# Kernel optimization log

Hardware: AMD Instinct MI355X
Metric: run time of the kernel (lower is better)

## Reference

```python
import jax, jax.numpy as jnp
import numpy as np

B, T, D, H = 8, 4096, 1024, 1024


def log_g(x):
    # log of g(x) = relu(x)+0.5 for x>=0, sigmoid(x) for x<0 (continuous at 0)
    return jnp.where(x >= 0, jnp.log(jax.nn.relu(x) + 0.5), -jax.nn.softplus(-x))


def setup_inputs() -> dict:
    key = jax.random.key(0)
    k0, k1, k2, k3, k4, k5 = jax.random.split(key, 6)
    s = 1.0 / np.sqrt(D)
    return {
        "x": jax.random.normal(k0, (B, T, D), jnp.float32),
        "h_0": jax.random.normal(k1, (B, H), jnp.float32),
        "Wz": jax.random.uniform(k2, (H, D), jnp.float32, -s, s),
        "bz": jax.random.uniform(k3, (H,), jnp.float32, -s, s),
        "Wh": jax.random.uniform(k4, (H, D), jnp.float32, -s, s),
        "bh": jax.random.uniform(k5, (H,), jnp.float32, -s, s),
    }


def reference(x, h_0, Wz, bz, Wh, bh):
    # gate pre-activation k: (B,T,H)
    k = jnp.einsum("btd,hd->bth", x, Wz) + bz
    log_z = -jax.nn.softplus(-k)        # log sigmoid(k)
    log_coeffs = -jax.nn.softplus(k)    # log (1 - sigmoid(k))
    log_h_0 = log_g(h_0)[:, None, :]    # (B,1,H)
    log_tilde_h = log_g(jnp.einsum("btd,hd->bth", x, Wh) + bh)
    log_values = jnp.concatenate([log_h_0, log_z + log_tilde_h], axis=1)  # (B,T+1,H)
    # parallel scan in log space
    a_star = jnp.pad(jnp.cumsum(log_coeffs, axis=1), ((0, 0), (1, 0), (0, 0)))
    log_h = a_star + jax.lax.cumlogsumexp(log_values - a_star, axis=1)
    h = jnp.exp(log_h)                  # (B,T+1,H)
    return h[:, -T:, :]
```

## Files before the change

kernel.cpp:

```cpp
#include <hip/hip_runtime.h>
#include <hip/hip_bf16.h>

#define Bb 8
#define Tt 4096
#define Dd 1024
#define Hh 1024
#define Mm (Bb * Tt)
#define NCHUNK 32
#define CLEN 128

typedef float f32x4 __attribute__((ext_vector_type(4)));
typedef short bf16x8 __attribute__((ext_vector_type(8)));

__device__ __forceinline__ unsigned f2bfu(float x) {
  unsigned u = __float_as_uint(x);
  return (u + 0x7fffu + ((u >> 16) & 1u)) >> 16;
}
__device__ __forceinline__ float bflo(unsigned u) { return __uint_as_float(u << 16); }
__device__ __forceinline__ float bfhi(unsigned u) { return __uint_as_float(u & 0xffff0000u); }

__global__ void cvt_kernel(const float* __restrict__ src, unsigned short* __restrict__ dst,
                           int n4) {
  int i = blockIdx.x * blockDim.x + threadIdx.x;
  int stride = gridDim.x * blockDim.x;
  for (; i < n4; i += stride) {
    float4 v = reinterpret_cast<const float4*>(src)[i];
    ushort4 o;
    o.x = (unsigned short)f2bfu(v.x);
    o.y = (unsigned short)f2bfu(v.y);
    o.z = (unsigned short)f2bfu(v.z);
    o.w = (unsigned short)f2bfu(v.w);
    reinterpret_cast<ushort4*>(dst)[i] = o;
  }
}

__device__ __forceinline__ void async16(const unsigned short* g, unsigned short* l) {
  __builtin_amdgcn_global_load_lds(
      (const __attribute__((address_space(1))) unsigned int*)g,
      (__attribute__((address_space(3))) unsigned int*)l, 16, 0, 0);
}

template <int MF0>
__device__ __forceinline__ void mfma16(const bf16x8 af[4], const bf16x8 bfr[4],
                                       f32x4 (&acc)[8][4]) {
#pragma unroll
  for (int i = 0; i < 4; ++i)
#pragma unroll
    for (int j = 0; j < 4; ++j)
      acc[MF0 + i][j] =
          __builtin_amdgcn_mfma_f32_16x16x32_bf16(af[i], bfr[j], acc[MF0 + i][j], 0, 0, 0);
}

__global__ void __launch_bounds__(512, 1) gemm_kernel(
    const unsigned short* __restrict__ xb,
    const unsigned short* __restrict__ wzb,
    const unsigned short* __restrict__ whb,
    const float* __restrict__ bz,
    const float* __restrict__ bh,
    unsigned int* __restrict__ P) {
  __shared__ unsigned short lds[65536];
  const int tid = threadIdx.x;
  const int wid = tid >> 6;
  const int wm = wid >> 2;
  const int wn = wid & 3;
  const int l = tid & 63, ln = l & 15, l4 = l >> 4;

  const int id = blockIdx.x;
  const int sw = (id & 7) * 128 + (id >> 3);
  const int mb = sw >> 3, nb = sw & 7;
  const int m0 = mb * 256, h0 = nb * 128;

  const int r0 = tid >> 2;
  const int chunk = ((tid & 3) - (tid >> 3)) & 3;
  const unsigned short* agp = xb + (size_t)(m0 + r0) * Dd + chunk * 8;
  const int sub16 = r0 >> 4;
  const int hrow0 = h0 + ((sub16 >> 1) << 4) + (r0 & 15);
  const unsigned short* bgp =
      ((sub16 & 1) ? whb : wzb) + (size_t)hrow0 * Dd + chunk * 8;
  const int dstoff = tid * 8;

  auto stA = [&](int reg) {
    unsigned short* d = &lds[reg * 8192] + dstoff;
    async16(agp, d);
    async16(agp + (size_t)128 * Dd, d + 4096);
    agp += 32;
  };
  auto stB = [&](int reg) {
    unsigned short* d = &lds[32768 + reg * 8192] + dstoff;
    async16(bgp, d);
    async16(bgp + (size_t)64 * Dd, d + 4096);
    bgp += 32;
  };

  int oA[8], oB[4];
#pragma unroll
  for (int mf = 0; mf < 8; ++mf) {
    const int row = wm * 128 + mf * 16 + ln;
    const int sl = (l4 + (row >> 1)) & 3;
    oA[mf] = row * 32 + sl * 8;
  }
#pragma unroll
  for (int nf = 0; nf < 4; ++nf) {
    const int row = wn * 64 + nf * 16 + ln;
    const int sl = (l4 + (row >> 1)) & 3;
    oB[nf] = row * 32 + sl * 8;
  }

  f32x4 acc[8][4];
#pragma unroll
  for (int i = 0; i < 8; ++i)
#pragma unroll
    for (int j = 0; j < 4; ++j) acc[i][j] = f32x4{0.f, 0.f, 0.f, 0.f};

  stA(0); stB(0);
  stA(1); stB(1);
  stA(2); stB(2);
  asm volatile("s_waitcnt vmcnt(4)" ::: "memory");
  __builtin_amdgcn_s_barrier();

#define PAIR(P, G)                                                        \
  {                                                                       \
    bf16x8 bfr[4];                                                        \
    const unsigned short* ba = &lds[(P) * 8192];                          \
    const unsigned short* bb = &lds[32768 + (P) * 8192];                  \
    bfr[0] = *(const bf16x8*)(bb + oB[0]);                                \
    bfr[1] = *(const bf16x8*)(bb + oB[1]);                                \
    bfr[2] = *(const bf16x8*)(bb + oB[2]);                                \
    bfr[3] = *(const bf16x8*)(bb + oB[3]);                                \
    {                                                                     \
      bf16x8 af[4];                                                       \
      af[0] = *(const bf16x8*)(ba + oA[0]);                               \
      af[1] = *(const bf16x8*)(ba + oA[1]);                               \
      af[2] = *(const bf16x8*)(ba + oA[2]);                               \
      af[3] = *(const bf16x8*)(ba + oA[3]);                               \
      stA(((P) + 3) & 3);                                                 \
      __builtin_amdgcn_s_barrier();                                       \
      __builtin_amdgcn_s_setprio(1);                                      \
      mfma16<0>(af, bfr, acc);                                            \
      __builtin_amdgcn_s_setprio(0);                                      \
      __builtin_amdgcn_s_barrier();                                       \
    }                                                                     \
    {                                                                     \
      bf16x8 af[4];                                                       \
      af[0] = *(const bf16x8*)(ba + oA[4]);                               \
      af[1] = *(const bf16x8*)(ba + oA[5]);                               \
      af[2] = *(const bf16x8*)(ba + oA[6]);                               \
      af[3] = *(const bf16x8*)(ba + oA[7]);                               \
      stB(((P) + 3) & 3);                                                 \
      __builtin_amdgcn_s_barrier();                                       \
      __builtin_amdgcn_s_setprio(1);                                      \
      mfma16<4>(af, bfr, acc);                                            \
      __builtin_amdgcn_s_setprio(0);                                      \
      if (G) asm volatile("s_waitcnt vmcnt(4)" ::: "memory");             \
      __builtin_amdgcn_s_barrier();                                       \
    }                                                                     \
  }

#pragma unroll 1
  for (int it = 0; it < 8; ++it) {
    PAIR(0, 0)
    PAIR(1, 1)
    PAIR(2, 0)
    PAIR(3, 1)
  }
#undef PAIR

  asm volatile("s_waitcnt vmcnt(0)" ::: "memory");

#pragma unroll
  for (int p = 0; p < 2; ++p) {
    const int hcol = h0 + (wn * 2 + p) * 16 + ln;
    const float bzv = bz[hcol];
    const float bhv = bh[hcol];
#pragma unroll
    for (int mf = 0; mf < 8; ++mf) {
#pragma unroll
      for (int q = 0; q < 4; ++q) {
        const int m = m0 + wm * 128 + mf * 16 + l4 * 4 + q;
        const float kv = acc[mf][2 * p][q] + bzv;
        const float pv = acc[mf][2 * p + 1][q] + bhv;
        const float ek = __expf(kv);
        const float a = 1.f / (1.f + ek);
        const float z = 1.f - a;
        const float g = (pv >= 0.f) ? (pv + 0.5f) : (1.f / (1.f + __expf(-pv)));
        const float c = z * g;
        P[(size_t)m * Hh + hcol] = f2bfu(a) | (f2bfu(c) << 16);
      }
    }
  }
}

__global__ void scan_pass1(const unsigned int* __restrict__ P,
                           float* __restrict__ Pp, float* __restrict__ Qq) {
  const int h = blockIdx.x * 256 + threadIdx.x;
  const int ch = blockIdx.y;
  const int b = blockIdx.z;
  const unsigned int* p = P + ((size_t)(b * Tt + ch * CLEN)) * Hh + h;
  float A = 1.f, Q = 0.f;
#pragma unroll 8
  for (int i = 0; i < CLEN; ++i) {
    const unsigned u = p[(size_t)i * Hh];
    Q = fmaf(bflo(u), Q, bfhi(u));
    A *= bflo(u);
  }
  const int idx = ch * (Bb * Hh) + b * Hh + h;
  Pp[idx] = A;
  Qq[idx] = Q;
}

__global__ void scan_pass2(const float* __restrict__ h0raw,
                           const float* __restrict__ Pp, const float* __restrict__ Qq,
                           float* __restrict__ Hinit) {
  const int bh = blockIdx.x * 256 + threadIdx.x;
  const float x = h0raw[bh];
  float hs = (x >= 0.f) ? (x + 0.5f) : (1.f / (1.f + __expf(-x)));
  for (int ch = 0; ch < NCHUNK; ++ch) {
    const int idx = ch * (Bb * Hh) + bh;
    Hinit[idx] = hs;
    hs = fmaf(Pp[idx], hs, Qq[idx]);
  }
}

__global__ void scan_pass3(const unsigned int* __restrict__ P,
                           const float* __restrict__ Hinit,
                           float* __restrict__ out) {
  const int h = blockIdx.x * 256 + threadIdx.x;
  const int ch = blockIdx.y;
  const int b = blockIdx.z;
  float hs = Hinit[ch * (Bb * Hh) + b * Hh + h];
  const size_t base = ((size_t)(b * Tt + ch * CLEN)) * Hh + h;
  const unsigned int* p = P + base;
  float* o = out + base;
#pragma unroll 8
  for (int i = 0; i < CLEN; ++i) {
    const unsigned u = p[(size_t)i * Hh];
    hs = fmaf(bflo(u), hs, bfhi(u));
    o[(size_t)i * Hh] = hs;
  }
}

extern "C" void kernel_launch(void* const* d_in, const int* in_sizes, int n_in,
                              void* d_out, int out_size, void* d_ws, size_t ws_size,
                              hipStream_t stream) {
  const float* x  = (const float*)d_in[0];
  const float* h0 = (const float*)d_in[1];
  const float* Wz = (const float*)d_in[2];
  const float* bz = (const float*)d_in[3];
  const float* Wh = (const float*)d_in[4];
  const float* bh = (const float*)d_in[5];
  float* out = (float*)d_out;

  char* ws = (char*)d_ws;
  unsigned short* xb  = (unsigned short*)(ws);
  unsigned short* wzb = (unsigned short*)(ws + 67108864);
  unsigned short* whb = (unsigned short*)(ws + 69206016);
  unsigned int*   P   = (unsigned int*)(ws + 71303168);
  float* Pp    = (float*)(ws + 205520896);
  float* Qq    = (float*)(ws + 206569472);
  float* Hinit = (float*)(ws + 207618048);

  cvt_kernel<<<4096, 256, 0, stream>>>(x, xb, Mm * Dd / 4);
  cvt_kernel<<<1024, 256, 0, stream>>>(Wz, wzb, Hh * Dd / 4);
  cvt_kernel<<<1024, 256, 0, stream>>>(Wh, whb, Hh * Dd / 4);

  gemm_kernel<<<1024, 512, 0, stream>>>(xb, wzb, whb, bz, bh, P);

  dim3 sgrid(Hh / 256, NCHUNK, Bb);
  scan_pass1<<<sgrid, 256, 0, stream>>>(P, Pp, Qq);
  scan_pass2<<<Bb * Hh / 256, 256, 0, stream>>>(h0, Pp, Qq, Hinit);
  scan_pass3<<<sgrid, 256, 0, stream>>>(P, Hinit, out);
}
```

Measured before the change: 273.2 us.

## Shrink GEMM tile to 128x128 with triple-buffered pipeline for higher occupancy

Halves the GEMM block tile along M (256 to 128 rows), cutting accumulators and LDS use (72KB) so several blocks can be resident per CU, and doubles the grid. The four-stage paired pipeline with split A/B staging is replaced by a simpler three-buffer loop with one barrier per K-step. This trades per-block operand reuse (more global/LDS traffic for the B tile) and a shallower prefetch for better latency hiding through occupancy.

```diff
diff --git a/kernel.cpp b/kernel.cpp
--- a/kernel.cpp
+++ b/kernel.cpp
@@ -40,25 +40,14 @@
       (__attribute__((address_space(3))) unsigned int*)l, 16, 0, 0);
 }
 
-template <int MF0>
-__device__ __forceinline__ void mfma16(const bf16x8 af[4], const bf16x8 bfr[4],
-                                       f32x4 (&acc)[8][4]) {
-#pragma unroll
-  for (int i = 0; i < 4; ++i)
-#pragma unroll
-    for (int j = 0; j < 4; ++j)
-      acc[MF0 + i][j] =
-          __builtin_amdgcn_mfma_f32_16x16x32_bf16(af[i], bfr[j], acc[MF0 + i][j], 0, 0, 0);
-}
-
-__global__ void __launch_bounds__(512, 1) gemm_kernel(
+__global__ void __launch_bounds__(512, 4) gemm_kernel(
     const unsigned short* __restrict__ xb,
     const unsigned short* __restrict__ wzb,
     const unsigned short* __restrict__ whb,
     const float* __restrict__ bz,
     const float* __restrict__ bh,
     unsigned int* __restrict__ P) {
-  __shared__ unsigned short lds[65536];
+  __shared__ unsigned short lds[36864];
   const int tid = threadIdx.x;
   const int wid = tid >> 6;
   const int wm = wid >> 2;
@@ -66,36 +55,32 @@
   const int l = tid & 63, ln = l & 15, l4 = l >> 4;
 
   const int id = blockIdx.x;
-  const int sw = (id & 7) * 128 + (id >> 3);
+  const int sw = (id & 7) * 256 + (id >> 3);
   const int mb = sw >> 3, nb = sw & 7;
-  const int m0 = mb * 256, h0 = nb * 128;
+  const int m0 = mb * 128, h0 = nb * 128;
 
   const int r0 = tid >> 2;
-  const int chunk = ((tid & 3) - (tid >> 3)) & 3;
+  const int chunk = ((tid & 3) - (r0 >> 1)) & 3;
   const unsigned short* agp = xb + (size_t)(m0 + r0) * Dd + chunk * 8;
   const int sub16 = r0 >> 4;
   const int hrow0 = h0 + ((sub16 >> 1) << 4) + (r0 & 15);
   const unsigned short* bgp =
       ((sub16 & 1) ? whb : wzb) + (size_t)hrow0 * Dd + chunk * 8;
-  const int dstoff = tid * 8;
-
-  auto stA = [&](int reg) {
-    unsigned short* d = &lds[reg * 8192] + dstoff;
-    async16(agp, d);
-    async16(agp + (size_t)128 * Dd, d + 4096);
+  const int ta = tid * 8;
+
+  auto stage = [&](int buf) {
+    unsigned short* d = &lds[buf * 12288];
+    async16(agp, d + ta);
+    async16(bgp, d + 4096 + ta);
+    async16(bgp + (size_t)64 * Dd, d + 8192 + ta);
     agp += 32;
-  };
-  auto stB = [&](int reg) {
-    unsigned short* d = &lds[32768 + reg * 8192] + dstoff;
-    async16(bgp, d);
-    async16(bgp + (size_t)64 * Dd, d + 4096);
     bgp += 32;
   };
 
-  int oA[8], oB[4];
-#pragma unroll
-  for (int mf = 0; mf < 8; ++mf) {
-    const int row = wm * 128 + mf * 16 + ln;
+  int oA[4], oB[4];
+#pragma unroll
+  for (int mf = 0; mf < 4; ++mf) {
+    const int row = wm * 64 + mf * 16 + ln;
     const int sl = (l4 + (row >> 1)) & 3;
     oA[mf] = row * 32 + sl * 8;
   }
@@ -103,67 +88,45 @@
   for (int nf = 0; nf < 4; ++nf) {
     const int row = wn * 64 + nf * 16 + ln;
     const int sl = (l4 + (row >> 1)) & 3;
-    oB[nf] = row * 32 + sl * 8;
-  }
-
-  f32x4 acc[8][4];
-#pragma unroll
-  for (int i = 0; i < 8; ++i)
+    oB[nf] = 4096 + row * 32 + sl * 8;
+  }
+
+  f32x4 acc[4][4];
+#pragma unroll
+  for (int i = 0; i < 4; ++i)
 #pragma unroll
     for (int j = 0; j < 4; ++j) acc[i][j] = f32x4{0.f, 0.f, 0.f, 0.f};
 
-  stA(0); stB(0);
-  stA(1); stB(1);
-  stA(2); stB(2);
-  asm volatile("s_waitcnt vmcnt(4)" ::: "memory");
-  __builtin_amdgcn_s_barrier();
-
-#define PAIR(P, G)                                                        \
-  {                                                                       \
-    bf16x8 bfr[4];                                                        \
-    const unsigned short* ba = &lds[(P) * 8192];                          \
-    const unsigned short* bb = &lds[32768 + (P) * 8192];                  \
-    bfr[0] = *(const bf16x8*)(bb + oB[0]);                                \
-    bfr[1] = *(const bf16x8*)(bb + oB[1]);                                \
-    bfr[2] = *(const bf16x8*)(bb + oB[2]);                                \
-    bfr[3] = *(const bf16x8*)(bb + oB[3]);                                \
-    {                                                                     \
-      bf16x8 af[4];                                                       \
-      af[0] = *(const bf16x8*)(ba + oA[0]);                               \
-      af[1] = *(const bf16x8*)(ba + oA[1]);                               \
-      af[2] = *(const bf16x8*)(ba + oA[2]);                               \
-      af[3] = *(const bf16x8*)(ba + oA[3]);                               \
-      stA(((P) + 3) & 3);                                                 \
-      __builtin_amdgcn_s_barrier();                                       \
-      __builtin_amdgcn_s_setprio(1);                                      \
-      mfma16<0>(af, bfr, acc);                                            \
-      __builtin_amdgcn_s_setprio(0);                                      \
-      __builtin_amdgcn_s_barrier();                                       \
-    }                                                                     \
-    {                                                                     \
-      bf16x8 af[4];                                                       \
-      af[0] = *(const bf16x8*)(ba + oA[4]);                               \
-      af[1] = *(const bf16x8*)(ba + oA[5]);                               \
-      af[2] = *(const bf16x8*)(ba + oA[6]);                               \
-      af[3] = *(const bf16x8*)(ba + oA[7]);                               \
-      stB(((P) + 3) & 3);                                                 \
-      __builtin_amdgcn_s_barrier();                                       \
-      __builtin_amdgcn_s_setprio(1);                                      \
-      mfma16<4>(af, bfr, acc);                                            \
-      __builtin_amdgcn_s_setprio(0);                                      \
-      if (G) asm volatile("s_waitcnt vmcnt(4)" ::: "memory");             \
-      __builtin_amdgcn_s_barrier();                                       \
-    }                                                                     \
-  }
-
+  stage(0);
+  stage(1);
+
+  int cur = 0, nxt = 2;
 #pragma unroll 1
-  for (int it = 0; it < 8; ++it) {
-    PAIR(0, 0)
-    PAIR(1, 1)
-    PAIR(2, 0)
-    PAIR(3, 1)
-  }
-#undef PAIR
+  for (int s = 0; s < 32; ++s) {
+    asm volatile("s_waitcnt vmcnt(3)" ::: "memory");
+    __builtin_amdgcn_s_barrier();
+    const unsigned short* bp = &lds[cur * 12288];
+    bf16x8 af[4], bf[4];
+    af[0] = *(const bf16x8*)(bp + oA[0]);
+    af[1] = *(const bf16x8*)(bp + oA[1]);
+    af[2] = *(const bf16x8*)(bp + oA[2]);
+    af[3] = *(const bf16x8*)(bp + oA[3]);
+    bf[0] = *(const bf16x8*)(bp + oB[0]);
+    bf[1] = *(const bf16x8*)(bp + oB[1]);
+    bf[2] = *(const bf16x8*)(bp + oB[2]);
+    bf[3] = *(const bf16x8*)(bp + oB[3]);
+    stage(nxt);
+    __builtin_amdgcn_s_setprio(1);
+#pragma unroll
+    for (int i = 0; i < 4; ++i)
+#pragma unroll
+      for (int j = 0; j < 4; ++j)
+        acc[i][j] =
+            __builtin_amdgcn_mfma_f32_16x16x32_bf16(af[i], bf[j], acc[i][j], 0, 0, 0);
+    __builtin_amdgcn_s_setprio(0);
+    cur = (cur + 1) == 3 ? 0 : cur + 1;
+    nxt = (nxt + 1) == 3 ? 0 : nxt + 1;
+  }
 
   asm volatile("s_waitcnt vmcnt(0)" ::: "memory");
 
@@ -173,10 +136,10 @@
     const float bzv = bz[hcol];
     const float bhv = bh[hcol];
 #pragma unroll
-    for (int mf = 0; mf < 8; ++mf) {
+    for (int mf = 0; mf < 4; ++mf) {
 #pragma unroll
       for (int q = 0; q < 4; ++q) {
-        const int m = m0 + wm * 128 + mf * 16 + l4 * 4 + q;
+        const int m = m0 + wm * 64 + mf * 16 + l4 * 4 + q;
         const float kv = acc[mf][2 * p][q] + bzv;
         const float pv = acc[mf][2 * p + 1][q] + bhv;
         const float ek = __expf(kv);
@@ -263,7 +226,7 @@
   cvt_kernel<<<1024, 256, 0, stream>>>(Wz, wzb, Hh * Dd / 4);
   cvt_kernel<<<1024, 256, 0, stream>>>(Wh, whb, Hh * Dd / 4);
 
-  gemm_kernel<<<1024, 512, 0, stream>>>(xb, wzb, whb, bz, bh, P);
+  gemm_kernel<<<2048, 512, 0, stream>>>(xb, wzb, whb, bz, bh, P);
 
   dim3 sgrid(Hh / 256, NCHUNK, Bb);
   scan_pass1<<<sgrid, 256, 0, stream>>>(P, Pp, Qq);
```

Result: no change. 277.7 us (+1.6%).
